# Optimization experiments

Measured on AMD Instinct MI355X. Metric: run time of the kernel, lower is better.

## Reference

```python
import jax, jax.numpy as jnp
import numpy as np

EMBED_DIM = 2048
NUM_HEADS = 16
NUM_KV_HEADS = 4
HEAD_DIM = EMBED_DIM // NUM_HEADS  # 128
N_REP = NUM_HEADS // NUM_KV_HEADS  # 4
B, S = 1, 4096


def setup_inputs() -> dict:
    key = jax.random.key(0)
    ks = jax.random.split(key, 10)
    sc = 1.0 / np.sqrt(EMBED_DIM)
    x = jax.random.normal(ks[0], (B, S, EMBED_DIM), dtype=jnp.float32)
    # causal mask: True above the diagonal -> positions to mask out
    mask = jnp.triu(jnp.ones((S, S), dtype=bool), k=1)[None, None, :, :]
    kv_dim = NUM_KV_HEADS * HEAD_DIM
    return {
        "x": x,
        "mask": mask,
        "wq_w": jax.random.normal(ks[1], (EMBED_DIM, EMBED_DIM), jnp.float32) * sc,
        "wq_b": jnp.zeros((EMBED_DIM,), jnp.float32),
        "wk_w": jax.random.normal(ks[2], (EMBED_DIM, kv_dim), jnp.float32) * sc,
        "wk_b": jnp.zeros((kv_dim,), jnp.float32),
        "wv_w": jax.random.normal(ks[3], (EMBED_DIM, kv_dim), jnp.float32) * sc,
        "wv_b": jnp.zeros((kv_dim,), jnp.float32),
        "wo_w": jax.random.normal(ks[4], (EMBED_DIM, EMBED_DIM), jnp.float32) * sc,
        "wo_b": jnp.zeros((EMBED_DIM,), jnp.float32),
    }


def reference(x, mask, wq_w, wq_b, wk_w, wk_b, wv_w, wv_b, wo_w, wo_b):
    b, s, _ = x.shape
    # projections
    q = (x @ wq_w + wq_b).reshape(b, s, NUM_HEADS, HEAD_DIM).transpose(0, 2, 1, 3)   # [b,h,s,d]
    k = (x @ wk_w + wk_b).reshape(b, s, NUM_KV_HEADS, HEAD_DIM).transpose(0, 2, 1, 3)  # [b,kv,s,d]
    v = (x @ wv_w + wv_b).reshape(b, s, NUM_KV_HEADS, HEAD_DIM).transpose(0, 2, 1, 3)
    # repeat_kv: expand kv heads to match q heads
    k_rep = jnp.repeat(k, N_REP, axis=1)  # [b,h,s,d]
    v_rep = jnp.repeat(v, N_REP, axis=1)
    scale = HEAD_DIM ** (-0.5)
    scores = jnp.einsum('bhqd,bhkd->bhqk', q, k_rep) * scale  # [b,h,s,s]
    scores = jnp.where(mask[:, :, -s:, :], -jnp.inf, scores)
    attn = jax.nn.softmax(scores, axis=-1)
    ctx = jnp.einsum('bhqk,bhkd->bhqd', attn, v_rep)
    ctx = ctx.transpose(0, 2, 1, 3).reshape(b, s, EMBED_DIM)
    out = ctx @ wo_w + wo_b
    return out
```

## Files before the change

### kernel.cpp

```cpp
#include <hip/hip_runtime.h>
#include <hip/hip_bf16.h>
#include <stdint.h>

#define S_LEN 4096
#define EMB   2048
#define KVD   512
#define HD    128
#define NH    16

typedef __attribute__((ext_vector_type(8))) short short8;
typedef __attribute__((ext_vector_type(4))) float f32x4;

#define AS1 __attribute__((address_space(1)))
#define AS3 __attribute__((address_space(3)))

__device__ __forceinline__ void gl2lds16(const void* g, void* l) {
  __builtin_amdgcn_global_load_lds((AS1 void*)g, (AS3 void*)l, 16, 0, 0);
}

__device__ __forceinline__ unsigned short f2bu(float f) {
  __hip_bfloat16 h = __float2bfloat16(f);
  unsigned short u;
  __builtin_memcpy(&u, &h, 2);
  return u;
}

__global__ void cvt_f32_bf16(const float* __restrict__ in, __hip_bfloat16* __restrict__ out, int n) {
  int i = blockIdx.x * blockDim.x + threadIdx.x;
  int stride = gridDim.x * blockDim.x;
  for (int idx = i * 4; idx < n; idx += stride * 4) {
    float4 f = *(const float4*)(in + idx);
    ushort4 u4 = make_ushort4(f2bu(f.x), f2bu(f.y), f2bu(f.z), f2bu(f.w));
    *reinterpret_cast<ushort4*>(out + idx) = u4;
  }
}

__global__ void transpose_f32_bf16(const float* __restrict__ W, __hip_bfloat16* __restrict__ WT,
                                   int K, int N) {
  __shared__ float t[32][33];
  int tx = threadIdx.x & 31, ty = threadIdx.x >> 5;
  int n0 = blockIdx.x * 32, k0 = blockIdx.y * 32;
  #pragma unroll
  for (int i = ty; i < 32; i += 8)
    t[i][tx] = W[(size_t)(k0 + i) * N + n0 + tx];
  __syncthreads();
  #pragma unroll
  for (int i = ty; i < 32; i += 8)
    WT[(size_t)(n0 + i) * K + k0 + tx] = __float2bfloat16(t[tx][i]);
}

__global__ void transpose_bf16(const __hip_bfloat16* __restrict__ W, __hip_bfloat16* __restrict__ WT,
                               int K, int N) {
  __shared__ __hip_bfloat16 t[32][33];
  int tx = threadIdx.x & 31, ty = threadIdx.x >> 5;
  int n0 = blockIdx.x * 32, k0 = blockIdx.y * 32;
  #pragma unroll
  for (int i = ty; i < 32; i += 8)
    t[i][tx] = W[(size_t)(k0 + i) * N + n0 + tx];
  __syncthreads();
  #pragma unroll
  for (int i = ty; i < 32; i += 8)
    WT[(size_t)(n0 + i) * K + k0 + tx] = t[tx][i];
}

template<int MODE>
__global__ __launch_bounds__(256, 2) void gemm_bt(
    const __hip_bfloat16* __restrict__ A, const __hip_bfloat16* __restrict__ Bt,
    int M, int N, int K,
    __hip_bfloat16* __restrict__ oQ, __hip_bfloat16* __restrict__ oK, __hip_bfloat16* __restrict__ oV,
    const float* __restrict__ bQ, const float* __restrict__ bK, const float* __restrict__ bV,
    float* __restrict__ oF, const float* __restrict__ bF) {
  __shared__ __align__(16) __hip_bfloat16 As[128 * 32];
  __shared__ __align__(16) __hip_bfloat16 Bs[128 * 32];
  const int tid = threadIdx.x, wid = tid >> 6, lane = tid & 63;
  const int g = lane >> 4, c = lane & 15;
  const int wm = wid >> 1, wn = wid & 1;
  const int m0 = blockIdx.y * 128, n0 = blockIdx.x * 128;
  const __hip_bfloat16* Ab = A + (size_t)m0 * K;
  const __hip_bfloat16* Bb = Bt + (size_t)n0 * K;
  f32x4 acc[4][4] = {};
  for (int k0 = 0; k0 < K; k0 += 32) {
    #pragma unroll
    for (int call = 0; call < 2; ++call) {
      int ci = wid * 128 + call * 64 + lane;
      gl2lds16(Ab + (size_t)(ci >> 2) * K + k0 + (ci & 3) * 8,
               (char*)As + (wid * 128 + call * 64) * 16);
      gl2lds16(Bb + (size_t)(ci >> 2) * K + k0 + (ci & 3) * 8,
               (char*)Bs + (wid * 128 + call * 64) * 16);
    }
    __syncthreads();
    short8 af[4], bfr[4];
    #pragma unroll
    for (int t = 0; t < 4; ++t) af[t]  = *(const short8*)&As[(wm * 64 + t * 16 + c) * 32 + g * 8];
    #pragma unroll
    for (int t = 0; t < 4; ++t) bfr[t] = *(const short8*)&Bs[(wn * 64 + t * 16 + c) * 32 + g * 8];
    #pragma unroll
    for (int i = 0; i < 4; ++i)
      #pragma unroll
      for (int j = 0; j < 4; ++j)
        acc[i][j] = __builtin_amdgcn_mfma_f32_16x16x32_bf16(af[i], bfr[j], acc[i][j], 0, 0, 0);
    __syncthreads();
  }
  #pragma unroll
  for (int i = 0; i < 4; ++i) {
    #pragma unroll
    for (int j = 0; j < 4; ++j) {
      int col = n0 + wn * 64 + j * 16 + c;
      #pragma unroll
      for (int r = 0; r < 4; ++r) {
        int row = m0 + wm * 64 + i * 16 + g * 4 + r;
        float v = acc[i][j][r];
        if (MODE == 0) {
          if (col < EMB) {
            oQ[(size_t)row * EMB + col] = __float2bfloat16((v + bQ[col]) * 0.08838834764831845f);
          } else if (col < EMB + KVD) {
            oK[(size_t)row * KVD + (col - EMB)] = __float2bfloat16(v + bK[col - EMB]);
          } else {
            oV[(size_t)row * KVD + (col - EMB - KVD)] = __float2bfloat16(v + bV[col - EMB - KVD]);
          }
        } else {
          oF[(size_t)row * EMB + col] = v + bF[col];
        }
      }
    }
  }
}


__device__ __forceinline__ void stage_kv(const __hip_bfloat16* __restrict__ Kb,
                                         const __hip_bfloat16* __restrict__ Vt,
                                         int kvh, int kv0, int wid,
                                         __hip_bfloat16* Ks, __hip_bfloat16* Vs) {
  const int lane = threadIdx.x & 63;
  #pragma unroll
  for (int call = 0; call < 4; ++call) {
    int ci = wid * 256 + call * 64 + lane;
    int r = ci >> 4, sl = ci & 15;
    gl2lds16(Kb + (size_t)(kv0 + r) * KVD + kvh * HD + ((sl ^ (r & 7)) << 3),
             (char*)Ks + (wid * 256 + call * 64) * 16);
    int d = ci >> 3, vs = ci & 7;
    gl2lds16(Vt + (size_t)(kvh * HD + d) * S_LEN + kv0 + ((vs ^ (d & 7)) << 3),
             (char*)Vs + (wid * 256 + call * 64) * 16);
  }
}

__device__ __forceinline__ void attn_qtile(
    int qb, int h, int kvh, int wid, int g, int c,
    const __hip_bfloat16* __restrict__ Q, const __hip_bfloat16* __restrict__ Kb,
    const __hip_bfloat16* __restrict__ Vt, __hip_bfloat16* __restrict__ ctx,
    __hip_bfloat16 (*Ks)[64 * 128], __hip_bfloat16 (*Vs)[128 * 64],
    __hip_bfloat16* Pw) {
  const int qrow = qb * 64 + wid * 16 + c;
  short8 qf[4];
  #pragma unroll
  for (int ks = 0; ks < 4; ++ks)
    qf[ks] = *(const short8*)&Q[(size_t)qrow * EMB + h * HD + ks * 32 + g * 8];
  f32x4 o[8] = {};
  float mreg[4] = {-1e30f, -1e30f, -1e30f, -1e30f};
  float lreg[4] = {0.f, 0.f, 0.f, 0.f};
  const int ntiles = qb + 1;
  stage_kv(Kb, Vt, kvh, 0, wid, Ks[0], Vs[0]);
  asm volatile("s_waitcnt vmcnt(0)" ::: "memory");
  __syncthreads();
  int buf = 0;
  for (int t = 0; t < ntiles; ++t) {
    const int kv0 = t * 64;
    if (t + 1 < ntiles)
      stage_kv(Kb, Vt, kvh, kv0 + 64, wid, Ks[buf ^ 1], Vs[buf ^ 1]);
    const char* Kbase = (const char*)Ks[buf];
    const char* Vbase = (const char*)Vs[buf];
    f32x4 sc[4] = {};
    #pragma unroll
    for (int ks = 0; ks < 4; ++ks) {
      #pragma unroll
      for (int nt = 0; nt < 4; ++nt) {
        int kvr = nt * 16 + c;
        int byt = ((kvr << 8) + (ks << 6) + (g << 4)) ^ ((kvr & 7) << 4);
        short8 kf = *(const short8*)(Kbase + byt);
        sc[nt] = __builtin_amdgcn_mfma_f32_16x16x32_bf16(qf[ks], kf, sc[nt], 0, 0, 0);
      }
    }
    if (t == ntiles - 1) {
      #pragma unroll
      for (int nt = 0; nt < 4; ++nt)
        #pragma unroll
        for (int r = 0; r < 4; ++r)
          if (kv0 + nt * 16 + c > qb * 64 + wid * 16 + g * 4 + r) sc[nt][r] = -1e30f;
    }
    float mx[4], rs[4], corr[4];
    #pragma unroll
    for (int r = 0; r < 4; ++r)
      mx[r] = fmaxf(fmaxf(sc[0][r], sc[1][r]), fmaxf(sc[2][r], sc[3][r]));
    #pragma unroll
    for (int d = 1; d < 16; d <<= 1)
      #pragma unroll
      for (int r = 0; r < 4; ++r) mx[r] = fmaxf(mx[r], __shfl_xor(mx[r], d, 64));
    #pragma unroll
    for (int r = 0; r < 4; ++r) {
      float mn = fmaxf(mreg[r], mx[r]);
      corr[r] = __expf(mreg[r] - mn);
      mreg[r] = mn;
    }
    #pragma unroll
    for (int nt = 0; nt < 4; ++nt)
      #pragma unroll
      for (int r = 0; r < 4; ++r) sc[nt][r] = __expf(sc[nt][r] - mreg[r]);
    #pragma unroll
    for (int r = 0; r < 4; ++r) rs[r] = sc[0][r] + sc[1][r] + sc[2][r] + sc[3][r];
    #pragma unroll
    for (int d = 1; d < 16; d <<= 1)
      #pragma unroll
      for (int r = 0; r < 4; ++r) rs[r] += __shfl_xor(rs[r], d, 64);
    #pragma unroll
    for (int r = 0; r < 4; ++r) lreg[r] = lreg[r] * corr[r] + rs[r];
    #pragma unroll
    for (int dt = 0; dt < 8; ++dt)
      #pragma unroll
      for (int r = 0; r < 4; ++r) o[dt][r] *= corr[r];
    #pragma unroll
    for (int nt = 0; nt < 4; ++nt)
      #pragma unroll
      for (int r = 0; r < 4; ++r)
        Pw[(g * 4 + r) * 72 + nt * 16 + c] = __float2bfloat16(sc[nt][r]);
    #pragma unroll
    for (int k2 = 0; k2 < 2; ++k2) {
      short8 pf = *(const short8*)&Pw[c * 72 + k2 * 32 + g * 8];
      #pragma unroll
      for (int dt = 0; dt < 8; ++dt) {
        int d = dt * 16 + c;
        int byt = ((d << 7) + (k2 << 6) + (g << 4)) ^ ((d & 7) << 4);
        short8 vf = *(const short8*)(Vbase + byt);
        o[dt] = __builtin_amdgcn_mfma_f32_16x16x32_bf16(pf, vf, o[dt], 0, 0, 0);
      }
    }
    asm volatile("s_waitcnt vmcnt(0)" ::: "memory");
    __syncthreads();
    buf ^= 1;
  }
  float inv[4];
  #pragma unroll
  for (int r = 0; r < 4; ++r) inv[r] = 1.f / lreg[r];
  #pragma unroll
  for (int dt = 0; dt < 8; ++dt)
    #pragma unroll
    for (int r = 0; r < 4; ++r)
      ctx[(size_t)(qb * 64 + wid * 16 + g * 4 + r) * EMB + h * HD + dt * 16 + c] =
          __float2bfloat16(o[dt][r] * inv[r]);
}

__global__ __launch_bounds__(256, 2) void attn_kernel(
    const __hip_bfloat16* __restrict__ Q, const __hip_bfloat16* __restrict__ Kb,
    const __hip_bfloat16* __restrict__ Vt, __hip_bfloat16* __restrict__ ctx) {
  __shared__ __align__(16) __hip_bfloat16 Ks[2][64 * 128];
  __shared__ __align__(16) __hip_bfloat16 Vs[2][128 * 64];
  __shared__ __align__(16) __hip_bfloat16 Ps[4][16 * 72];
  const int h = blockIdx.y, i = blockIdx.x;
  const int kvh = h >> 2;
  const int wid = threadIdx.x >> 6, lane = threadIdx.x & 63;
  const int g = lane >> 4, c = lane & 15;
  attn_qtile(i, h, kvh, wid, g, c, Q, Kb, Vt, ctx, Ks, Vs, Ps[wid]);
  attn_qtile(63 - i, h, kvh, wid, g, c, Q, Kb, Vt, ctx, Ks, Vs, Ps[wid]);
}

extern "C" void kernel_launch(void* const* d_in, const int* in_sizes, int n_in,
                              void* d_out, int out_size, void* d_ws, size_t ws_size,
                              hipStream_t stream) {
  const float* x  = (const float*)d_in[0];
  const float* wq = (const float*)d_in[2];
  const float* qb = (const float*)d_in[3];
  const float* wk = (const float*)d_in[4];
  const float* kb = (const float*)d_in[5];
  const float* wv = (const float*)d_in[6];
  const float* vb = (const float*)d_in[7];
  const float* wo = (const float*)d_in[8];
  const float* ob = (const float*)d_in[9];

  char* ws = (char*)d_ws;
  __hip_bfloat16* x_bf  = (__hip_bfloat16*)(ws);
  __hip_bfloat16* wqkvT = (__hip_bfloat16*)(ws + 16777216);
  __hip_bfloat16* woT   = (__hip_bfloat16*)(ws + 29360128);
  __hip_bfloat16* q_bf  = (__hip_bfloat16*)(ws + 37748736);
  __hip_bfloat16* k_bf  = (__hip_bfloat16*)(ws + 54525952);
  __hip_bfloat16* v_bf  = (__hip_bfloat16*)(ws + 58720256);
  __hip_bfloat16* vT    = (__hip_bfloat16*)(ws + 62914560);
  __hip_bfloat16* ctx   = (__hip_bfloat16*)(ws + 67108864);

  cvt_f32_bf16<<<2048, 256, 0, stream>>>(x, x_bf, S_LEN * EMB);
  transpose_f32_bf16<<<dim3(64, 64), 256, 0, stream>>>(wq, wqkvT, EMB, EMB);
  transpose_f32_bf16<<<dim3(16, 64), 256, 0, stream>>>(wk, wqkvT + (size_t)EMB * EMB, EMB, KVD);
  transpose_f32_bf16<<<dim3(16, 64), 256, 0, stream>>>(wv, wqkvT + (size_t)(EMB + KVD) * EMB, EMB, KVD);
  transpose_f32_bf16<<<dim3(64, 64), 256, 0, stream>>>(wo, woT, EMB, EMB);

  gemm_bt<0><<<dim3(24, 32), 256, 0, stream>>>(x_bf, wqkvT, S_LEN, 3072, EMB,
      q_bf, k_bf, v_bf, qb, kb, vb, nullptr, nullptr);

  transpose_bf16<<<dim3(16, 128), 256, 0, stream>>>(v_bf, vT, S_LEN, KVD);

  attn_kernel<<<dim3(32, NH), 256, 0, stream>>>(q_bf, k_bf, vT, ctx);

  gemm_bt<1><<<dim3(16, 32), 256, 0, stream>>>(ctx, woT, S_LEN, EMB, EMB,
      nullptr, nullptr, nullptr, nullptr, nullptr, nullptr, (float*)d_out, ob);
}
```

Measured before the change: 454.0 us.

## Fuse weight transposes, write V transposed from GEMM, lazy-rescale exp2 softmax

Merges the four weight transpose launches into one 3D-grid kernel. The QKV GEMM epilogue now writes V directly in transposed layout, which removes a separate transpose kernel. In attention, Q is prescaled by log2(e)/sqrt(d) so exp2 can be used. The running max and rescale are updated only when some row max grows past a threshold of 8. The per-tile row-sum shuffles are also deferred to a single reduction at the end. The risks are scattered, uncoalesced stores for the V transpose in the GEMM epilogue and slightly different numerics from the lazy rescaling.

```diff
diff --git a/kernel.cpp b/kernel.cpp
--- a/kernel.cpp
+++ b/kernel.cpp
@@ -1,6 +1,7 @@
 #include <hip/hip_runtime.h>
 #include <hip/hip_bf16.h>
 #include <stdint.h>
+#include <math.h>
 
 #define S_LEN 4096
 #define EMB   2048
@@ -16,6 +17,14 @@
 
 __device__ __forceinline__ void gl2lds16(const void* g, void* l) {
   __builtin_amdgcn_global_load_lds((AS1 void*)g, (AS3 void*)l, 16, 0, 0);
+}
+
+__device__ __forceinline__ float fexp2(float x) {
+#if __has_builtin(__builtin_amdgcn_exp2f)
+  return __builtin_amdgcn_exp2f(x);
+#else
+  return exp2f(x);
+#endif
 }
 
 __device__ __forceinline__ unsigned short f2bu(float f) {
@@ -35,39 +44,35 @@
   }
 }
 
-__global__ void transpose_f32_bf16(const float* __restrict__ W, __hip_bfloat16* __restrict__ WT,
-                                   int K, int N) {
+__global__ void transpose_weights(const float* __restrict__ wq, const float* __restrict__ wk,
+                                  const float* __restrict__ wv, const float* __restrict__ wo,
+                                  __hip_bfloat16* __restrict__ wqkvT, __hip_bfloat16* __restrict__ woT) {
+  const int z = blockIdx.z;
+  const float* W;
+  __hip_bfloat16* WT;
+  int N;
+  if (z == 0)      { W = wq; WT = wqkvT;                              N = EMB; }
+  else if (z == 1) { W = wo; WT = woT;                                N = EMB; }
+  else if (z == 2) { W = wk; WT = wqkvT + (size_t)EMB * EMB;          N = KVD; }
+  else             { W = wv; WT = wqkvT + (size_t)(EMB + KVD) * EMB;  N = KVD; }
+  int n0 = blockIdx.x * 32, k0 = blockIdx.y * 32;
+  if (n0 >= N) return;
   __shared__ float t[32][33];
   int tx = threadIdx.x & 31, ty = threadIdx.x >> 5;
-  int n0 = blockIdx.x * 32, k0 = blockIdx.y * 32;
   #pragma unroll
   for (int i = ty; i < 32; i += 8)
     t[i][tx] = W[(size_t)(k0 + i) * N + n0 + tx];
   __syncthreads();
   #pragma unroll
   for (int i = ty; i < 32; i += 8)
-    WT[(size_t)(n0 + i) * K + k0 + tx] = __float2bfloat16(t[tx][i]);
-}
-
-__global__ void transpose_bf16(const __hip_bfloat16* __restrict__ W, __hip_bfloat16* __restrict__ WT,
-                               int K, int N) {
-  __shared__ __hip_bfloat16 t[32][33];
-  int tx = threadIdx.x & 31, ty = threadIdx.x >> 5;
-  int n0 = blockIdx.x * 32, k0 = blockIdx.y * 32;
-  #pragma unroll
-  for (int i = ty; i < 32; i += 8)
-    t[i][tx] = W[(size_t)(k0 + i) * N + n0 + tx];
-  __syncthreads();
-  #pragma unroll
-  for (int i = ty; i < 32; i += 8)
-    WT[(size_t)(n0 + i) * K + k0 + tx] = t[tx][i];
+    WT[(size_t)(n0 + i) * EMB + k0 + tx] = __float2bfloat16(t[tx][i]);
 }
 
 template<int MODE>
 __global__ __launch_bounds__(256, 2) void gemm_bt(
     const __hip_bfloat16* __restrict__ A, const __hip_bfloat16* __restrict__ Bt,
     int M, int N, int K,
-    __hip_bfloat16* __restrict__ oQ, __hip_bfloat16* __restrict__ oK, __hip_bfloat16* __restrict__ oV,
+    __hip_bfloat16* __restrict__ oQ, __hip_bfloat16* __restrict__ oK, __hip_bfloat16* __restrict__ oVt,
     const float* __restrict__ bQ, const float* __restrict__ bK, const float* __restrict__ bV,
     float* __restrict__ oF, const float* __restrict__ bF) {
   __shared__ __align__(16) __hip_bfloat16 As[128 * 32];
@@ -112,11 +117,12 @@
         float v = acc[i][j][r];
         if (MODE == 0) {
           if (col < EMB) {
-            oQ[(size_t)row * EMB + col] = __float2bfloat16((v + bQ[col]) * 0.08838834764831845f);
+            oQ[(size_t)row * EMB + col] = __float2bfloat16((v + bQ[col]) * 0.12751743f);
           } else if (col < EMB + KVD) {
             oK[(size_t)row * KVD + (col - EMB)] = __float2bfloat16(v + bK[col - EMB]);
           } else {
-            oV[(size_t)row * KVD + (col - EMB - KVD)] = __float2bfloat16(v + bV[col - EMB - KVD]);
+            int d = col - EMB - KVD;
+            oVt[(size_t)d * S_LEN + row] = __float2bfloat16(v + bV[d]);
           }
         } else {
           oF[(size_t)row * EMB + col] = v + bF[col];
@@ -187,36 +193,39 @@
         for (int r = 0; r < 4; ++r)
           if (kv0 + nt * 16 + c > qb * 64 + wid * 16 + g * 4 + r) sc[nt][r] = -1e30f;
     }
-    float mx[4], rs[4], corr[4];
+    float pmax[4];
     #pragma unroll
     for (int r = 0; r < 4; ++r)
-      mx[r] = fmaxf(fmaxf(sc[0][r], sc[1][r]), fmaxf(sc[2][r], sc[3][r]));
-    #pragma unroll
-    for (int d = 1; d < 16; d <<= 1)
-      #pragma unroll
-      for (int r = 0; r < 4; ++r) mx[r] = fmaxf(mx[r], __shfl_xor(mx[r], d, 64));
-    #pragma unroll
-    for (int r = 0; r < 4; ++r) {
-      float mn = fmaxf(mreg[r], mx[r]);
-      corr[r] = __expf(mreg[r] - mn);
-      mreg[r] = mn;
+      pmax[r] = fmaxf(fmaxf(sc[0][r], sc[1][r]), fmaxf(sc[2][r], sc[3][r]));
+    bool ok = (pmax[0] <= mreg[0] + 8.f) & (pmax[1] <= mreg[1] + 8.f) &
+              (pmax[2] <= mreg[2] + 8.f) & (pmax[3] <= mreg[3] + 8.f);
+    if (!__all((int)ok)) {
+      float mx[4], corr[4];
+      #pragma unroll
+      for (int r = 0; r < 4; ++r) mx[r] = pmax[r];
+      #pragma unroll
+      for (int d = 1; d < 16; d <<= 1)
+        #pragma unroll
+        for (int r = 0; r < 4; ++r) mx[r] = fmaxf(mx[r], __shfl_xor(mx[r], d, 64));
+      #pragma unroll
+      for (int r = 0; r < 4; ++r) {
+        float mn = fmaxf(mreg[r], mx[r]);
+        corr[r] = fexp2(mreg[r] - mn);
+        mreg[r] = mn;
+        lreg[r] *= corr[r];
+      }
+      #pragma unroll
+      for (int dt = 0; dt < 8; ++dt)
+        #pragma unroll
+        for (int r = 0; r < 4; ++r) o[dt][r] *= corr[r];
     }
     #pragma unroll
     for (int nt = 0; nt < 4; ++nt)
       #pragma unroll
-      for (int r = 0; r < 4; ++r) sc[nt][r] = __expf(sc[nt][r] - mreg[r]);
-    #pragma unroll
-    for (int r = 0; r < 4; ++r) rs[r] = sc[0][r] + sc[1][r] + sc[2][r] + sc[3][r];
-    #pragma unroll
-    for (int d = 1; d < 16; d <<= 1)
-      #pragma unroll
-      for (int r = 0; r < 4; ++r) rs[r] += __shfl_xor(rs[r], d, 64);
-    #pragma unroll
-    for (int r = 0; r < 4; ++r) lreg[r] = lreg[r] * corr[r] + rs[r];
-    #pragma unroll
-    for (int dt = 0; dt < 8; ++dt)
-      #pragma unroll
-      for (int r = 0; r < 4; ++r) o[dt][r] *= corr[r];
+      for (int r = 0; r < 4; ++r) sc[nt][r] = fexp2(sc[nt][r] - mreg[r]);
+    #pragma unroll
+    for (int r = 0; r < 4; ++r)
+      lreg[r] += sc[0][r] + sc[1][r] + sc[2][r] + sc[3][r];
     #pragma unroll
     for (int nt = 0; nt < 4; ++nt)
       #pragma unroll
@@ -237,6 +246,10 @@
     __syncthreads();
     buf ^= 1;
   }
+  #pragma unroll
+  for (int d = 1; d < 16; d <<= 1)
+    #pragma unroll
+    for (int r = 0; r < 4; ++r) lreg[r] += __shfl_xor(lreg[r], d, 64);
   float inv[4];
   #pragma unroll
   for (int r = 0; r < 4; ++r) inv[r] = 1.f / lreg[r];
@@ -281,20 +294,14 @@
   __hip_bfloat16* woT   = (__hip_bfloat16*)(ws + 29360128);
   __hip_bfloat16* q_bf  = (__hip_bfloat16*)(ws + 37748736);
   __hip_bfloat16* k_bf  = (__hip_bfloat16*)(ws + 54525952);
-  __hip_bfloat16* v_bf  = (__hip_bfloat16*)(ws + 58720256);
   __hip_bfloat16* vT    = (__hip_bfloat16*)(ws + 62914560);
   __hip_bfloat16* ctx   = (__hip_bfloat16*)(ws + 67108864);
 
   cvt_f32_bf16<<<2048, 256, 0, stream>>>(x, x_bf, S_LEN * EMB);
-  transpose_f32_bf16<<<dim3(64, 64), 256, 0, stream>>>(wq, wqkvT, EMB, EMB);
-  transpose_f32_bf16<<<dim3(16, 64), 256, 0, stream>>>(wk, wqkvT + (size_t)EMB * EMB, EMB, KVD);
-  transpose_f32_bf16<<<dim3(16, 64), 256, 0, stream>>>(wv, wqkvT + (size_t)(EMB + KVD) * EMB, EMB, KVD);
-  transpose_f32_bf16<<<dim3(64, 64), 256, 0, stream>>>(wo, woT, EMB, EMB);
+  transpose_weights<<<dim3(64, 64, 4), 256, 0, stream>>>(wq, wk, wv, wo, wqkvT, woT);
 
   gemm_bt<0><<<dim3(24, 32), 256, 0, stream>>>(x_bf, wqkvT, S_LEN, 3072, EMB,
-      q_bf, k_bf, v_bf, qb, kb, vb, nullptr, nullptr);
-
-  transpose_bf16<<<dim3(16, 128), 256, 0, stream>>>(v_bf, vT, S_LEN, KVD);
+      q_bf, k_bf, vT, qb, kb, vb, nullptr, nullptr);
 
   attn_kernel<<<dim3(32, NH), 256, 0, stream>>>(q_bf, k_bf, vT, ctx);
 
```

New measurement: 414.3 us. 8.7% less time.
